# Optimization experiments

Measured on AMD Instinct MI355X. Metric: run time of the kernel, lower is better.

Reference implementation:

```python
import jax, jax.numpy as jnp
import numpy as np

HIDDEN = 1024
VOCAB = 50257
MAXLEN = 64


def setup_inputs() -> dict:
    key = jax.random.key(0)
    ks = jax.random.split(key, 16)
    s = 0.02
    return {
        "token": jax.random.randint(ks[0], (1,), 0, VOCAB, dtype=jnp.int64),
        "hidden": jax.random.normal(ks[1], (1, 1, HIDDEN), dtype=jnp.float32),
        "encoder_outputs": jax.random.normal(ks[2], (MAXLEN, HIDDEN), dtype=jnp.float32),
        "emb": jax.random.normal(ks[3], (VOCAB, HIDDEN), dtype=jnp.float32) * s,
        "attn_W": jax.random.normal(ks[4], (MAXLEN, 2 * HIDDEN), dtype=jnp.float32) * s,
        "attn_b": jnp.zeros((MAXLEN,), dtype=jnp.float32),
        "comb_W": jax.random.normal(ks[5], (HIDDEN, 2 * HIDDEN), dtype=jnp.float32) * s,
        "comb_b": jnp.zeros((HIDDEN,), dtype=jnp.float32),
        "W_ih": jax.random.normal(ks[6], (3 * HIDDEN, HIDDEN), dtype=jnp.float32) * s,
        "W_hh": jax.random.normal(ks[7], (3 * HIDDEN, HIDDEN), dtype=jnp.float32) * s,
        "b_ih": jnp.zeros((3 * HIDDEN,), dtype=jnp.float32),
        "b_hh": jnp.zeros((3 * HIDDEN,), dtype=jnp.float32),
        "out_W": jax.random.normal(ks[8], (VOCAB, HIDDEN), dtype=jnp.float32) * s,
        "out_b": jnp.zeros((VOCAB,), dtype=jnp.float32),
    }


def reference(token, hidden, encoder_outputs, emb, attn_W, attn_b,
              comb_W, comb_b, W_ih, W_hh, b_ih, b_hh, out_W, out_b):
    # embedded: [1, H] (dropout is identity in eval mode)
    embedded = emb[token].reshape(1, -1)
    h0 = hidden[0]  # [1, H]
    # attention over the encoder window: [1, MAXLEN]
    scores = jnp.concatenate([embedded, h0], axis=1) @ attn_W.T + attn_b
    attn_weights = jax.nn.softmax(scores, axis=1)
    # context: [1, H]
    attn_applied = attn_weights @ encoder_outputs
    # combine + relu: [1, H]
    x = jnp.concatenate([embedded, attn_applied], axis=1) @ comb_W.T + comb_b
    x = jax.nn.relu(x)
    # single GRU step (PyTorch gate math)
    gi = x @ W_ih.T + b_ih    # [1, 3H]
    gh = h0 @ W_hh.T + b_hh   # [1, 3H]
    i_r, i_z, i_n = jnp.split(gi, 3, axis=1)
    h_r, h_z, h_n = jnp.split(gh, 3, axis=1)
    r = jax.nn.sigmoid(i_r + h_r)
    z = jax.nn.sigmoid(i_z + h_z)
    n = jnp.tanh(i_n + r * h_n)
    h_new = (1.0 - z) * n + z * h0  # [1, H]
    logits = h_new @ out_W.T + out_b  # [1, VOCAB]
    return logits, h_new[None, :, :], attn_weights
```

## Files before the change

### kernel.cpp

```cpp
#include <hip/hip_runtime.h>
#include <math.h>

#define HIDDEN 1024
#define VOCAB  50257
#define MAXLEN 64

__device__ __forceinline__ float wave_reduce_sum(float v) {
    #pragma unroll
    for (int off = 32; off > 0; off >>= 1)
        v += __shfl_down(v, off, 64);
    return v;
}

__global__ __launch_bounds__(1024) void k_prelude(
    const int* __restrict__ token,
    const float* __restrict__ emb,
    const float* __restrict__ hidden,
    const float* __restrict__ enc,
    const float* __restrict__ attn_W,
    const float* __restrict__ attn_b,
    float* __restrict__ ws_ctx,
    float* __restrict__ out_attn)
{
    __shared__ float sc[MAXLEN];
    __shared__ float wsm[MAXLEN];
    const int t = threadIdx.x;
    const int w = t >> 6, lane = t & 63;
    const float4* e4 = (const float4*)(emb + (size_t)token[0] * HIDDEN);
    const float4* h4 = (const float4*)hidden;

    #pragma unroll
    for (int r = 0; r < 4; ++r) {
        const int m = w * 4 + r;
        const float4* Wr = (const float4*)(attn_W + (size_t)m * 2 * HIDDEN);
        float acc = 0.f;
        #pragma unroll
        for (int it = 0; it < 8; ++it) {
            int i = lane + it * 64;
            float4 a = Wr[i];
            float4 c = (i < 256) ? e4[i] : h4[i - 256];
            acc += a.x * c.x + a.y * c.y + a.z * c.z + a.w * c.w;
        }
        acc = wave_reduce_sum(acc);
        if (lane == 0) sc[m] = acc + attn_b[m];
    }
    __syncthreads();

    if (w == 0) {
        float s = sc[lane];
        float mx = s;
        #pragma unroll
        for (int off = 32; off > 0; off >>= 1) mx = fmaxf(mx, __shfl_xor(mx, off, 64));
        float e = expf(s - mx);
        float sum = e;
        #pragma unroll
        for (int off = 32; off > 0; off >>= 1) sum += __shfl_xor(sum, off, 64);
        float wv = e / sum;
        wsm[lane] = wv;
        out_attn[lane] = wv;
    }
    __syncthreads();

    float acc = 0.f;
    #pragma unroll 8
    for (int m = 0; m < MAXLEN; ++m)
        acc += wsm[m] * enc[(size_t)m * HIDDEN + t];
    ws_ctx[t] = acc;
}

__global__ void k_combine(const int* __restrict__ token,
                          const float* __restrict__ emb,
                          const float* __restrict__ ws_ctx,
                          const float* __restrict__ comb_W,
                          const float* __restrict__ comb_b,
                          float* __restrict__ ws_x) {
    const int wid = threadIdx.x >> 6, lane = threadIdx.x & 63;
    const int j = blockIdx.x * 4 + wid;
    const float* erow = emb + (size_t)token[0] * HIDDEN;
    const float4* Wrow = (const float4*)(comb_W + (size_t)j * 2 * HIDDEN);
    float acc = 0.f;
    #pragma unroll
    for (int it = 0; it < 8; ++it) {
        int i = lane + it * 64;
        float4 w4 = Wrow[i];
        int k = i * 4;
        const float* src = (k < HIDDEN) ? (erow + k) : (ws_ctx + k - HIDDEN);
        float4 c4 = *(const float4*)src;
        acc += w4.x * c4.x + w4.y * c4.y + w4.z * c4.z + w4.w * c4.w;
    }
    acc = wave_reduce_sum(acc);
    if (lane == 0) ws_x[j] = fmaxf(acc + comb_b[j], 0.f);
}

__global__ __launch_bounds__(384) void k_gru(
    const float* __restrict__ ws_x,
    const float* __restrict__ hidden,
    const float* __restrict__ W_ih,
    const float* __restrict__ W_hh,
    const float* __restrict__ b_ih,
    const float* __restrict__ b_hh,
    float* __restrict__ ws_h,
    float* __restrict__ out_h)
{
    __shared__ float dval[6];
    const int j = blockIdx.x;
    const int q = threadIdx.x >> 6, lane = threadIdx.x & 63;
    const float* row = (q < 3)
        ? (W_ih + (size_t)(j + q * HIDDEN) * HIDDEN)
        : (W_hh + (size_t)(j + (q - 3) * HIDDEN) * HIDDEN);
    const float* vec = (q < 3) ? ws_x : hidden;
    const float4* W4 = (const float4*)row;
    const float4* v4 = (const float4*)vec;
    float acc = 0.f;
    #pragma unroll
    for (int it = 0; it < 4; ++it) {
        int i = lane + it * 64;
        float4 a = W4[i];
        float4 b = v4[i];
        acc += a.x * b.x + a.y * b.y + a.z * b.z + a.w * b.w;
    }
    acc = wave_reduce_sum(acc);
    if (lane == 0) dval[q] = acc;
    __syncthreads();
    if (threadIdx.x == 0) {
        float i_r = dval[0] + b_ih[j];
        float i_z = dval[1] + b_ih[j + HIDDEN];
        float i_n = dval[2] + b_ih[j + 2 * HIDDEN];
        float h_r = dval[3] + b_hh[j];
        float h_z = dval[4] + b_hh[j + HIDDEN];
        float h_n = dval[5] + b_hh[j + 2 * HIDDEN];
        float r = 1.f / (1.f + expf(-(i_r + h_r)));
        float z = 1.f / (1.f + expf(-(i_z + h_z)));
        float n = tanhf(i_n + r * h_n);
        float h0v = hidden[j];
        float hn = (1.f - z) * n + z * h0v;
        ws_h[j] = hn;
        out_h[j] = hn;
    }
}

__global__ __launch_bounds__(256) void k_logits(
    const float* __restrict__ ws_h,
    const float* __restrict__ out_W,
    const float* __restrict__ out_b,
    float* __restrict__ out_logits)
{
    const int t = threadIdx.x;
    const int wid = t >> 6, lane = t & 63;
    const float4* h4 = (const float4*)ws_h;
    const float4 hv0 = h4[lane];
    const float4 hv1 = h4[lane + 64];
    const float4 hv2 = h4[lane + 128];
    const float4 hv3 = h4[lane + 192];

    const int base = blockIdx.x * 16 + wid * 4;
    float acc[4];
    #pragma unroll
    for (int r = 0; r < 4; ++r) {
        int v = base + r;
        if (v > VOCAB - 1) v = VOCAB - 1;
        const float4* W = (const float4*)(out_W + (size_t)v * HIDDEN);
        float4 a0 = W[lane];
        float4 a1 = W[lane + 64];
        float4 a2 = W[lane + 128];
        float4 a3 = W[lane + 192];
        float s;
        s  = a0.x * hv0.x + a0.y * hv0.y + a0.z * hv0.z + a0.w * hv0.w;
        s += a1.x * hv1.x + a1.y * hv1.y + a1.z * hv1.z + a1.w * hv1.w;
        s += a2.x * hv2.x + a2.y * hv2.y + a2.z * hv2.z + a2.w * hv2.w;
        s += a3.x * hv3.x + a3.y * hv3.y + a3.z * hv3.z + a3.w * hv3.w;
        acc[r] = s;
    }
    #pragma unroll
    for (int r = 0; r < 4; ++r)
        acc[r] = wave_reduce_sum(acc[r]);
    if (lane == 0) {
        #pragma unroll
        for (int r = 0; r < 4; ++r) {
            const int v = base + r;
            if (v < VOCAB) out_logits[v] = acc[r] + out_b[v];
        }
    }
}

extern "C" void kernel_launch(void* const* d_in, const int* in_sizes, int n_in,
                              void* d_out, int out_size, void* d_ws, size_t ws_size,
                              hipStream_t stream) {
    const int*   token  = (const int*)d_in[0];
    const float* hidden = (const float*)d_in[1];
    const float* enc    = (const float*)d_in[2];
    const float* emb    = (const float*)d_in[3];
    const float* attn_W = (const float*)d_in[4];
    const float* attn_b = (const float*)d_in[5];
    const float* comb_W = (const float*)d_in[6];
    const float* comb_b = (const float*)d_in[7];
    const float* W_ih   = (const float*)d_in[8];
    const float* W_hh   = (const float*)d_in[9];
    const float* b_ih   = (const float*)d_in[10];
    const float* b_hh   = (const float*)d_in[11];
    const float* out_W  = (const float*)d_in[12];
    const float* out_b  = (const float*)d_in[13];

    float* out = (float*)d_out;
    float* out_logits = out;
    float* out_h      = out + VOCAB;
    float* out_attn   = out + VOCAB + HIDDEN;

    float* ws = (float*)d_ws;
    float* ws_ctx = ws;
    float* ws_x   = ws + 1024;
    float* ws_h   = ws + 2048;

    k_prelude<<<1, 1024, 0, stream>>>(token, emb, hidden, enc, attn_W, attn_b,
                                      ws_ctx, out_attn);
    k_combine<<<HIDDEN / 4, 256, 0, stream>>>(token, emb, ws_ctx, comb_W, comb_b, ws_x);
    k_gru<<<HIDDEN, 384, 0, stream>>>(ws_x, hidden, W_ih, W_hh, b_ih, b_hh, ws_h, out_h);
    k_logits<<<(VOCAB + 15) / 16, 256, 0, stream>>>(ws_h, out_W, out_b, out_logits);
}
```

Baseline: 57.63 us.

## Hoist input-independent matvecs into a wide front kernel and split attention softmax

Moves the W_hh·h0 GRU matvec and the embedding half of the combine matvec, both of which depend only on the inputs, into a new wide k_front kernel alongside the attention scores. The old single-block prelude is replaced by a multi-block launch plus a small 16-block softmax/context kernel. This takes work off the serial critical path: the previous prelude ran on one block, and the combine and GRU kernels each carried twice the weight traffic. It adds one kernel launch and extra workspace round trips for the partial results.

```diff
diff --git a/kernel.cpp b/kernel.cpp
--- a/kernel.cpp
+++ b/kernel.cpp
@@ -12,26 +12,26 @@
     return v;
 }
 
-__global__ __launch_bounds__(1024) void k_prelude(
+__global__ __launch_bounds__(256) void k_front(
     const int* __restrict__ token,
     const float* __restrict__ emb,
     const float* __restrict__ hidden,
-    const float* __restrict__ enc,
     const float* __restrict__ attn_W,
     const float* __restrict__ attn_b,
-    float* __restrict__ ws_ctx,
-    float* __restrict__ out_attn)
-{
-    __shared__ float sc[MAXLEN];
-    __shared__ float wsm[MAXLEN];
-    const int t = threadIdx.x;
-    const int w = t >> 6, lane = t & 63;
-    const float4* e4 = (const float4*)(emb + (size_t)token[0] * HIDDEN);
-    const float4* h4 = (const float4*)hidden;
-
-    #pragma unroll
-    for (int r = 0; r < 4; ++r) {
-        const int m = w * 4 + r;
+    const float* __restrict__ W_hh,
+    const float* __restrict__ b_hh,
+    const float* __restrict__ comb_W,
+    float* __restrict__ ws_sc,
+    float* __restrict__ ws_gh,
+    float* __restrict__ ws_cemb)
+{
+    const int b = blockIdx.x;
+    const int wid = threadIdx.x >> 6, lane = threadIdx.x & 63;
+
+    if (b < 16) {
+        const int m = b * 4 + wid;
+        const float4* e4 = (const float4*)(emb + (size_t)token[0] * HIDDEN);
+        const float4* h4 = (const float4*)hidden;
         const float4* Wr = (const float4*)(attn_W + (size_t)m * 2 * HIDDEN);
         float acc = 0.f;
         #pragma unroll
@@ -42,75 +42,104 @@
             acc += a.x * c.x + a.y * c.y + a.z * c.z + a.w * c.w;
         }
         acc = wave_reduce_sum(acc);
-        if (lane == 0) sc[m] = acc + attn_b[m];
-    }
+        if (lane == 0) ws_sc[m] = acc + attn_b[m];
+    } else if (b < 784) {
+        const int row = (b - 16) * 4 + wid;
+        const float4* Wr = (const float4*)(W_hh + (size_t)row * HIDDEN);
+        const float4* h4 = (const float4*)hidden;
+        float acc = 0.f;
+        #pragma unroll
+        for (int it = 0; it < 4; ++it) {
+            int i = lane + it * 64;
+            float4 a = Wr[i];
+            float4 c = h4[i];
+            acc += a.x * c.x + a.y * c.y + a.z * c.z + a.w * c.w;
+        }
+        acc = wave_reduce_sum(acc);
+        if (lane == 0) ws_gh[row] = acc + b_hh[row];
+    } else {
+        const int j = (b - 784) * 4 + wid;
+        const float4* Wr = (const float4*)(comb_W + (size_t)j * 2 * HIDDEN);
+        const float4* e4 = (const float4*)(emb + (size_t)token[0] * HIDDEN);
+        float acc = 0.f;
+        #pragma unroll
+        for (int it = 0; it < 4; ++it) {
+            int i = lane + it * 64;
+            float4 a = Wr[i];
+            float4 c = e4[i];
+            acc += a.x * c.x + a.y * c.y + a.z * c.z + a.w * c.w;
+        }
+        acc = wave_reduce_sum(acc);
+        if (lane == 0) ws_cemb[j] = acc;
+    }
+}
+
+__global__ __launch_bounds__(64) void k_smctx(
+    const float* __restrict__ ws_sc,
+    const float* __restrict__ enc,
+    float* __restrict__ ws_ctx,
+    float* __restrict__ out_attn)
+{
+    __shared__ float wsm[MAXLEN];
+    const int t = threadIdx.x;
+    float s = ws_sc[t];
+    float mx = s;
+    #pragma unroll
+    for (int off = 32; off > 0; off >>= 1) mx = fmaxf(mx, __shfl_xor(mx, off, 64));
+    float e = expf(s - mx);
+    float sum = e;
+    #pragma unroll
+    for (int off = 32; off > 0; off >>= 1) sum += __shfl_xor(sum, off, 64);
+    float wv = e / sum;
+    wsm[t] = wv;
+    if (blockIdx.x == 0) out_attn[t] = wv;
     __syncthreads();
 
-    if (w == 0) {
-        float s = sc[lane];
-        float mx = s;
-        #pragma unroll
-        for (int off = 32; off > 0; off >>= 1) mx = fmaxf(mx, __shfl_xor(mx, off, 64));
-        float e = expf(s - mx);
-        float sum = e;
-        #pragma unroll
-        for (int off = 32; off > 0; off >>= 1) sum += __shfl_xor(sum, off, 64);
-        float wv = e / sum;
-        wsm[lane] = wv;
-        out_attn[lane] = wv;
-    }
-    __syncthreads();
-
+    const int col = blockIdx.x * 64 + t;
     float acc = 0.f;
     #pragma unroll 8
     for (int m = 0; m < MAXLEN; ++m)
-        acc += wsm[m] * enc[(size_t)m * HIDDEN + t];
-    ws_ctx[t] = acc;
-}
-
-__global__ void k_combine(const int* __restrict__ token,
-                          const float* __restrict__ emb,
-                          const float* __restrict__ ws_ctx,
-                          const float* __restrict__ comb_W,
-                          const float* __restrict__ comb_b,
-                          float* __restrict__ ws_x) {
+        acc += wsm[m] * enc[(size_t)m * HIDDEN + col];
+    ws_ctx[col] = acc;
+}
+
+__global__ __launch_bounds__(256) void k_combine(
+    const float* __restrict__ ws_ctx,
+    const float* __restrict__ ws_cemb,
+    const float* __restrict__ comb_W,
+    const float* __restrict__ comb_b,
+    float* __restrict__ ws_x)
+{
     const int wid = threadIdx.x >> 6, lane = threadIdx.x & 63;
     const int j = blockIdx.x * 4 + wid;
-    const float* erow = emb + (size_t)token[0] * HIDDEN;
-    const float4* Wrow = (const float4*)(comb_W + (size_t)j * 2 * HIDDEN);
+    const float4* Wr = (const float4*)(comb_W + (size_t)j * 2 * HIDDEN + HIDDEN);
+    const float4* c4 = (const float4*)ws_ctx;
     float acc = 0.f;
     #pragma unroll
-    for (int it = 0; it < 8; ++it) {
+    for (int it = 0; it < 4; ++it) {
         int i = lane + it * 64;
-        float4 w4 = Wrow[i];
-        int k = i * 4;
-        const float* src = (k < HIDDEN) ? (erow + k) : (ws_ctx + k - HIDDEN);
-        float4 c4 = *(const float4*)src;
-        acc += w4.x * c4.x + w4.y * c4.y + w4.z * c4.z + w4.w * c4.w;
+        float4 a = Wr[i];
+        float4 c = c4[i];
+        acc += a.x * c.x + a.y * c.y + a.z * c.z + a.w * c.w;
     }
     acc = wave_reduce_sum(acc);
-    if (lane == 0) ws_x[j] = fmaxf(acc + comb_b[j], 0.f);
-}
-
-__global__ __launch_bounds__(384) void k_gru(
+    if (lane == 0) ws_x[j] = fmaxf(acc + ws_cemb[j] + comb_b[j], 0.f);
+}
+
+__global__ __launch_bounds__(192) void k_gru(
     const float* __restrict__ ws_x,
+    const float* __restrict__ ws_gh,
     const float* __restrict__ hidden,
     const float* __restrict__ W_ih,
-    const float* __restrict__ W_hh,
     const float* __restrict__ b_ih,
-    const float* __restrict__ b_hh,
     float* __restrict__ ws_h,
     float* __restrict__ out_h)
 {
-    __shared__ float dval[6];
+    __shared__ float dval[3];
     const int j = blockIdx.x;
     const int q = threadIdx.x >> 6, lane = threadIdx.x & 63;
-    const float* row = (q < 3)
-        ? (W_ih + (size_t)(j + q * HIDDEN) * HIDDEN)
-        : (W_hh + (size_t)(j + (q - 3) * HIDDEN) * HIDDEN);
-    const float* vec = (q < 3) ? ws_x : hidden;
-    const float4* W4 = (const float4*)row;
-    const float4* v4 = (const float4*)vec;
+    const float4* W4 = (const float4*)(W_ih + (size_t)(j + q * HIDDEN) * HIDDEN);
+    const float4* v4 = (const float4*)ws_x;
     float acc = 0.f;
     #pragma unroll
     for (int it = 0; it < 4; ++it) {
@@ -126,9 +155,9 @@
         float i_r = dval[0] + b_ih[j];
         float i_z = dval[1] + b_ih[j + HIDDEN];
         float i_n = dval[2] + b_ih[j + 2 * HIDDEN];
-        float h_r = dval[3] + b_hh[j];
-        float h_z = dval[4] + b_hh[j + HIDDEN];
-        float h_n = dval[5] + b_hh[j + 2 * HIDDEN];
+        float h_r = ws_gh[j];
+        float h_z = ws_gh[j + HIDDEN];
+        float h_n = ws_gh[j + 2 * HIDDEN];
         float r = 1.f / (1.f + expf(-(i_r + h_r)));
         float z = 1.f / (1.f + expf(-(i_z + h_z)));
         float n = tanhf(i_n + r * h_n);
@@ -207,13 +236,17 @@
     float* out_attn   = out + VOCAB + HIDDEN;
 
     float* ws = (float*)d_ws;
-    float* ws_ctx = ws;
-    float* ws_x   = ws + 1024;
-    float* ws_h   = ws + 2048;
-
-    k_prelude<<<1, 1024, 0, stream>>>(token, emb, hidden, enc, attn_W, attn_b,
-                                      ws_ctx, out_attn);
-    k_combine<<<HIDDEN / 4, 256, 0, stream>>>(token, emb, ws_ctx, comb_W, comb_b, ws_x);
-    k_gru<<<HIDDEN, 384, 0, stream>>>(ws_x, hidden, W_ih, W_hh, b_ih, b_hh, ws_h, out_h);
+    float* ws_sc   = ws;
+    float* ws_gh   = ws + 64;
+    float* ws_cemb = ws + 3136;
+    float* ws_ctx  = ws + 4160;
+    float* ws_x    = ws + 5184;
+    float* ws_h    = ws + 6208;
+
+    k_front<<<1040, 256, 0, stream>>>(token, emb, hidden, attn_W, attn_b,
+                                      W_hh, b_hh, comb_W, ws_sc, ws_gh, ws_cemb);
+    k_smctx<<<16, 64, 0, stream>>>(ws_sc, enc, ws_ctx, out_attn);
+    k_combine<<<HIDDEN / 4, 256, 0, stream>>>(ws_ctx, ws_cemb, comb_W, comb_b, ws_x);
+    k_gru<<<HIDDEN, 192, 0, stream>>>(ws_x, ws_gh, hidden, W_ih, b_ih, ws_h, out_h);
     k_logits<<<(VOCAB + 15) / 16, 256, 0, stream>>>(ws_h, out_W, out_b, out_logits);
 }
```

After: 52.04 us (median of 2 runs). 1.11x faster.
